# Kernel optimization log

Hardware: AMD Instinct MI355X
Metric: run time of the kernel (lower is better)

## Reference

```python
import jax, jax.numpy as jnp
import numpy as np

NOISE_STD = 0.05
ALPHA = 0.2

B, T, I, H, O, R = 64, 1024, 8, 512, 2, 2


def setup_inputs() -> dict:
    key = jax.random.key(0)
    ks = jax.random.split(key, 6)
    return {
        "input": jax.random.normal(ks[0], (B, T, I), dtype=jnp.float32),
        "noise": jax.random.normal(ks[1], (B, T, H), dtype=jnp.float32),
        "wi": jax.random.normal(ks[2], (I, H), dtype=jnp.float32),
        "si": jnp.ones((I,), dtype=jnp.float32),
        "m": jax.random.normal(ks[3], (H, R), dtype=jnp.float32),
        "n": jax.random.normal(ks[4], (H, R), dtype=jnp.float32),
        "wo": jax.random.normal(ks[5], (H, O), dtype=jnp.float32) * 4.0,
        "so": jnp.ones((O,), dtype=jnp.float32),
        "h0": jnp.zeros((H,), dtype=jnp.float32),
    }


def reference(input, noise, wi, si, m, n, wo, so, h0):
    batch, seq_len, _ = input.shape
    hidden = m.shape[0]
    wi_full = wi * si[:, None]          # (I, H)
    wo_full = wo * so                   # (H, O)
    # Precompute input projection for all timesteps: (B, T, H)
    inp_proj = jnp.einsum('bti,ih->bth', input, wi_full)
    h_init = jnp.broadcast_to(h0, (batch, hidden))
    r_init = jnp.tanh(h_init)

    def step(carry, xs):
        h, r = carry
        nz, p = xs  # (B, H) each
        rec = (r @ n) @ m.T / hidden    # rank-r recurrent drive
        h = h + NOISE_STD * nz + ALPHA * (-h + rec + p)
        r = jnp.tanh(h)
        out = r @ wo_full / hidden      # (B, O)
        return (h, r), (out, h)

    xs = (jnp.swapaxes(noise, 0, 1), jnp.swapaxes(inp_proj, 0, 1))  # time-major
    _, (output, traj) = jax.lax.scan(step, (h_init, r_init), xs)
    return jnp.swapaxes(output, 0, 1), jnp.swapaxes(traj, 0, 1)
```

## Files before the change

kernel.cpp:

```cpp
#include <hip/hip_runtime.h>
#include <cstddef>

constexpr int B = 64, T = 1024, I = 8, H = 512, O = 2;
constexpr float ALPHA = 0.2f;
constexpr float NOISE_STD = 0.05f;

constexpr int PF = 8;

template <int CTRL>
__device__ __forceinline__ float dpp_add(float x) {
    int y = __builtin_amdgcn_update_dpp(0, __float_as_int(x), CTRL, 0xF, 0xF, true);
    return x + __int_as_float(y);
}

__device__ __forceinline__ float wave_sum_to_lane63(float x) {
    x = dpp_add<0x111>(x);
    x = dpp_add<0x112>(x);
    x = dpp_add<0x114>(x);
    x = dpp_add<0x118>(x);
    x = dpp_add<0x142>(x);
    x = dpp_add<0x143>(x);
    return x;
}

__device__ __forceinline__ float fast_tanh(float x) {
    float z = __builtin_amdgcn_exp2f(x * 2.885390081777927f);
    return fmaf(-2.0f, __builtin_amdgcn_rcpf(z + 1.0f), 1.0f);
}

__global__ __launch_bounds__(256)
void rnn_fused4_kernel(const float* __restrict__ input,
                       const float* __restrict__ noise,
                       const float* __restrict__ wi,
                       const float* __restrict__ si,
                       const float* __restrict__ m,
                       const float* __restrict__ n,
                       const float* __restrict__ wo,
                       const float* __restrict__ so,
                       const float* __restrict__ h0,
                       float* __restrict__ out,
                       float* __restrict__ traj)
{
    const int b    = blockIdx.x;
    const int w    = threadIdx.x >> 6;
    const int lane = threadIdx.x & 63;
    const int j0   = w * 128 + 2 * lane;

    __shared__ float  xin[T * I];
    __shared__ float4 part[2][4];

    {
        const float4* src = (const float4*)(input + (size_t)b * T * I);
        float4*       dst = (float4*)xin;
#pragma unroll
        for (int i = 0; i < (T * I / 4) / 256; ++i)
            dst[threadIdx.x + 256 * i] = src[threadIdx.x + 256 * i];
    }
    __syncthreads();

    constexpr float RS  = ALPHA / (float)H;
    constexpr float OMA = 1.0f - ALPHA;
    const float so0 = so[0] / (float)H;
    const float so1 = so[1] / (float)H;

    const float4 mv = *(const float4*)(m + 2 * j0);
    const float4 nv = *(const float4*)(n + 2 * j0);
    const float4 wv = *(const float4*)(wo + 2 * j0);
    const float mm0[2] = {mv.x * RS, mv.z * RS};
    const float mm1[2] = {mv.y * RS, mv.w * RS};
    const float nn0[2] = {nv.x, nv.z};
    const float nn1[2] = {nv.y, nv.w};
    const float ww0[2] = {wv.x, wv.z};
    const float ww1[2] = {wv.y, wv.w};

    float wif[I][2];
#pragma unroll
    for (int i = 0; i < I; ++i) {
        wif[i][0] = wi[i * H + j0]     * si[i];
        wif[i][1] = wi[i * H + j0 + 1] * si[i];
    }

    const float2 h0v = *(const float2*)(h0 + j0);
    float h[2] = {h0v.x, h0v.y};
    float r[2] = {tanhf(h[0]), tanhf(h[1])};

    const float* pn   = noise + (size_t)b * T * H + j0;
    float*       pt   = traj  + (size_t)b * T * H + j0;
    float*       pout = out   + (size_t)b * T * O;

    float2 ring[PF];
#pragma unroll
    for (int u = 0; u < PF; ++u) ring[u] = *(const float2*)(pn + (size_t)u * H);

    static_assert(T % PF == 0, "T must be a multiple of PF");

    for (int tb = 0; tb < T; tb += PF) {
#pragma unroll
        for (int u = 0; u < PF; ++u) {
            const int t = tb + u;

            const float4 xa = *(const float4*)(xin + t * I);
            const float4 xb = *(const float4*)(xin + t * I + 4);

            float pa0 = fmaf(r[1], nn0[1], r[0] * nn0[0]);
            float pa1 = fmaf(r[1], nn1[1], r[0] * nn1[0]);
            float po0 = fmaf(r[1], ww0[1], r[0] * ww0[0]);
            float po1 = fmaf(r[1], ww1[1], r[0] * ww1[0]);

            const float2 nz = ring[u];
            if (t + PF < T) ring[u] = *(const float2*)(pn + (size_t)(t + PF) * H);

            pa0 = wave_sum_to_lane63(pa0);
            pa1 = wave_sum_to_lane63(pa1);
            po0 = wave_sum_to_lane63(po0);
            po1 = wave_sum_to_lane63(po1);

            const float x0 = xa.x, x1 = xa.y, x2 = xa.z, x3 = xa.w;
            const float x4 = xb.x, x5 = xb.y, x6 = xb.z, x7 = xb.w;
            float acc0 = x0 * wif[0][0], acc1 = x0 * wif[0][1];
            acc0 = fmaf(x1, wif[1][0], acc0); acc1 = fmaf(x1, wif[1][1], acc1);
            acc0 = fmaf(x2, wif[2][0], acc0); acc1 = fmaf(x2, wif[2][1], acc1);
            acc0 = fmaf(x3, wif[3][0], acc0); acc1 = fmaf(x3, wif[3][1], acc1);
            acc0 = fmaf(x4, wif[4][0], acc0); acc1 = fmaf(x4, wif[4][1], acc1);
            acc0 = fmaf(x5, wif[5][0], acc0); acc1 = fmaf(x5, wif[5][1], acc1);
            acc0 = fmaf(x6, wif[6][0], acc0); acc1 = fmaf(x6, wif[6][1], acc1);
            acc0 = fmaf(x7, wif[7][0], acc0); acc1 = fmaf(x7, wif[7][1], acc1);
            const float dv0 = fmaf(NOISE_STD, nz.x, ALPHA * acc0);
            const float dv1 = fmaf(NOISE_STD, nz.y, ALPHA * acc1);
            const float pre0 = fmaf(h[0], OMA, dv0);
            const float pre1 = fmaf(h[1], OMA, dv1);

            if (lane == 63) part[t & 1][w] = make_float4(pa0, pa1, po0, po1);

            __builtin_amdgcn_sched_barrier(0);
            asm volatile("s_waitcnt lgkmcnt(0)" ::: "memory");
            __builtin_amdgcn_s_barrier();
            __builtin_amdgcn_sched_barrier(0);

            const float4 q0 = part[t & 1][0];
            const float4 q1 = part[t & 1][1];
            const float4 q2 = part[t & 1][2];
            const float4 q3 = part[t & 1][3];
            const float a0 = (q0.x + q1.x) + (q2.x + q3.x);
            const float a1 = (q0.y + q1.y) + (q2.y + q3.y);

            if (t > 0 && threadIdx.x == 63) {
                const float o0 = (q0.z + q1.z) + (q2.z + q3.z);
                const float o1 = (q0.w + q1.w) + (q2.w + q3.w);
                *(float2*)(pout + (size_t)(t - 1) * O) =
                    make_float2(o0 * so0, o1 * so1);
            }

            h[0] = fmaf(a1, mm1[0], fmaf(a0, mm0[0], pre0));
            h[1] = fmaf(a1, mm1[1], fmaf(a0, mm0[1], pre1));
            r[0] = fast_tanh(h[0]);
            r[1] = fast_tanh(h[1]);

            *(float2*)(pt + (size_t)t * H) = make_float2(h[0], h[1]);
        }
    }

    {
        float po0 = fmaf(r[1], ww0[1], r[0] * ww0[0]);
        float po1 = fmaf(r[1], ww1[1], r[0] * ww1[0]);
        po0 = wave_sum_to_lane63(po0);
        po1 = wave_sum_to_lane63(po1);
        if (lane == 63) part[0][w] = make_float4(po0, po1, 0.f, 0.f);
        __syncthreads();
        if (threadIdx.x == 0) {
            const float4 q0 = part[0][0];
            const float4 q1 = part[0][1];
            const float4 q2 = part[0][2];
            const float4 q3 = part[0][3];
            const float o0 = (q0.x + q1.x) + (q2.x + q3.x);
            const float o1 = (q0.y + q1.y) + (q2.y + q3.y);
            *(float2*)(pout + (size_t)(T - 1) * O) =
                make_float2(o0 * so0, o1 * so1);
        }
    }
}

extern "C" void kernel_launch(void* const* d_in, const int* in_sizes, int n_in,
                              void* d_out, int out_size, void* d_ws, size_t ws_size,
                              hipStream_t stream) {
    const float* input = (const float*)d_in[0];
    const float* noise = (const float*)d_in[1];
    const float* wi    = (const float*)d_in[2];
    const float* si    = (const float*)d_in[3];
    const float* m     = (const float*)d_in[4];
    const float* n     = (const float*)d_in[5];
    const float* wo    = (const float*)d_in[6];
    const float* so    = (const float*)d_in[7];
    const float* h0    = (const float*)d_in[8];

    float* out  = (float*)d_out;
    float* traj = (float*)d_out + (size_t)B * T * O;

    (void)d_ws; (void)ws_size;

    rnn_fused4_kernel<<<B, 256, 0, stream>>>(input, noise, wi, si,
                                             m, n, wo, so, h0, out, traj);
}
```

Before: 560.9 us.

## Process two batch rows per block to share per-step barrier latency

Each 256-thread block now advances two independent batch recurrences in lockstep, so the grid has half as many blocks. The wave reductions, LDS partial exchange and single per-step barrier are shared by two chains, which adds instruction-level parallelism to hide the latency of the serial time loop. In exchange, each block does double the per-step ALU and memory work, uses more registers, and fewer CUs are active. Clamped prefetch indices remove branches, and the output for step t-1 is written from a wrapped index; the bogus write at t=0 lands on T-1 and is overwritten after the loop.

```diff
diff --git a/kernel.cpp b/kernel.cpp
--- a/kernel.cpp
+++ b/kernel.cpp
@@ -6,6 +6,7 @@
 constexpr float NOISE_STD = 0.05f;
 
 constexpr int PF = 8;
+constexpr int NB = 2;
 
 template <int CTRL>
 __device__ __forceinline__ float dpp_add(float x) {
@@ -29,31 +30,31 @@
 }
 
 __global__ __launch_bounds__(256)
-void rnn_fused4_kernel(const float* __restrict__ input,
-                       const float* __restrict__ noise,
-                       const float* __restrict__ wi,
-                       const float* __restrict__ si,
-                       const float* __restrict__ m,
-                       const float* __restrict__ n,
-                       const float* __restrict__ wo,
-                       const float* __restrict__ so,
-                       const float* __restrict__ h0,
-                       float* __restrict__ out,
-                       float* __restrict__ traj)
+void rnn_dual_kernel(const float* __restrict__ input,
+                     const float* __restrict__ noise,
+                     const float* __restrict__ wi,
+                     const float* __restrict__ si,
+                     const float* __restrict__ m,
+                     const float* __restrict__ n,
+                     const float* __restrict__ wo,
+                     const float* __restrict__ so,
+                     const float* __restrict__ h0,
+                     float* __restrict__ out,
+                     float* __restrict__ traj)
 {
-    const int b    = blockIdx.x;
+    const int b0   = blockIdx.x * NB;
     const int w    = threadIdx.x >> 6;
     const int lane = threadIdx.x & 63;
     const int j0   = w * 128 + 2 * lane;
 
-    __shared__ float  xin[T * I];
-    __shared__ float4 part[2][4];
+    __shared__ float  xin[NB * T * I];
+    __shared__ float4 part[2][NB][4];
 
     {
-        const float4* src = (const float4*)(input + (size_t)b * T * I);
+        const float4* src = (const float4*)(input + (size_t)b0 * T * I);
         float4*       dst = (float4*)xin;
 #pragma unroll
-        for (int i = 0; i < (T * I / 4) / 256; ++i)
+        for (int i = 0; i < (NB * T * I / 4) / 256; ++i)
             dst[threadIdx.x + 256 * i] = src[threadIdx.x + 256 * i];
     }
     __syncthreads();
@@ -81,101 +82,146 @@
     }
 
     const float2 h0v = *(const float2*)(h0 + j0);
-    float h[2] = {h0v.x, h0v.y};
-    float r[2] = {tanhf(h[0]), tanhf(h[1])};
-
-    const float* pn   = noise + (size_t)b * T * H + j0;
-    float*       pt   = traj  + (size_t)b * T * H + j0;
-    float*       pout = out   + (size_t)b * T * O;
-
-    float2 ring[PF];
-#pragma unroll
-    for (int u = 0; u < PF; ++u) ring[u] = *(const float2*)(pn + (size_t)u * H);
+    float h[NB][2], r[NB][2];
+#pragma unroll
+    for (int q = 0; q < NB; ++q) {
+        h[q][0] = h0v.x;        h[q][1] = h0v.y;
+        r[q][0] = tanhf(h0v.x); r[q][1] = tanhf(h0v.y);
+    }
+
+    const float* pn[NB];
+    float*       pt[NB];
+    float*       pout[NB];
+#pragma unroll
+    for (int q = 0; q < NB; ++q) {
+        pn[q]   = noise + (size_t)(b0 + q) * T * H + j0;
+        pt[q]   = traj  + (size_t)(b0 + q) * T * H + j0;
+        pout[q] = out   + (size_t)(b0 + q) * T * O;
+    }
+
+    float2 ring[NB][PF];
+#pragma unroll
+    for (int u = 0; u < PF; ++u)
+#pragma unroll
+        for (int q = 0; q < NB; ++q)
+            ring[q][u] = *(const float2*)(pn[q] + (size_t)u * H);
 
     static_assert(T % PF == 0, "T must be a multiple of PF");
 
     for (int tb = 0; tb < T; tb += PF) {
 #pragma unroll
         for (int u = 0; u < PF; ++u) {
-            const int t = tb + u;
-
-            const float4 xa = *(const float4*)(xin + t * I);
-            const float4 xb = *(const float4*)(xin + t * I + 4);
-
-            float pa0 = fmaf(r[1], nn0[1], r[0] * nn0[0]);
-            float pa1 = fmaf(r[1], nn1[1], r[0] * nn1[0]);
-            float po0 = fmaf(r[1], ww0[1], r[0] * ww0[0]);
-            float po1 = fmaf(r[1], ww1[1], r[0] * ww1[0]);
-
-            const float2 nz = ring[u];
-            if (t + PF < T) ring[u] = *(const float2*)(pn + (size_t)(t + PF) * H);
-
-            pa0 = wave_sum_to_lane63(pa0);
-            pa1 = wave_sum_to_lane63(pa1);
-            po0 = wave_sum_to_lane63(po0);
-            po1 = wave_sum_to_lane63(po1);
-
-            const float x0 = xa.x, x1 = xa.y, x2 = xa.z, x3 = xa.w;
-            const float x4 = xb.x, x5 = xb.y, x6 = xb.z, x7 = xb.w;
-            float acc0 = x0 * wif[0][0], acc1 = x0 * wif[0][1];
-            acc0 = fmaf(x1, wif[1][0], acc0); acc1 = fmaf(x1, wif[1][1], acc1);
-            acc0 = fmaf(x2, wif[2][0], acc0); acc1 = fmaf(x2, wif[2][1], acc1);
-            acc0 = fmaf(x3, wif[3][0], acc0); acc1 = fmaf(x3, wif[3][1], acc1);
-            acc0 = fmaf(x4, wif[4][0], acc0); acc1 = fmaf(x4, wif[4][1], acc1);
-            acc0 = fmaf(x5, wif[5][0], acc0); acc1 = fmaf(x5, wif[5][1], acc1);
-            acc0 = fmaf(x6, wif[6][0], acc0); acc1 = fmaf(x6, wif[6][1], acc1);
-            acc0 = fmaf(x7, wif[7][0], acc0); acc1 = fmaf(x7, wif[7][1], acc1);
-            const float dv0 = fmaf(NOISE_STD, nz.x, ALPHA * acc0);
-            const float dv1 = fmaf(NOISE_STD, nz.y, ALPHA * acc1);
-            const float pre0 = fmaf(h[0], OMA, dv0);
-            const float pre1 = fmaf(h[1], OMA, dv1);
-
-            if (lane == 63) part[t & 1][w] = make_float4(pa0, pa1, po0, po1);
+            const int t  = tb + u;
+            const int tn = (t + PF < T) ? (t + PF) : (T - 1);
+
+            float pa0[NB], pa1[NB], po0[NB], po1[NB];
+#pragma unroll
+            for (int q = 0; q < NB; ++q) {
+                pa0[q] = fmaf(r[q][1], nn0[1], r[q][0] * nn0[0]);
+                pa1[q] = fmaf(r[q][1], nn1[1], r[q][0] * nn1[0]);
+                po0[q] = fmaf(r[q][1], ww0[1], r[q][0] * ww0[0]);
+                po1[q] = fmaf(r[q][1], ww1[1], r[q][0] * ww1[0]);
+            }
+
+            float2 nz[NB];
+#pragma unroll
+            for (int q = 0; q < NB; ++q) {
+                nz[q]      = ring[q][u];
+                ring[q][u] = *(const float2*)(pn[q] + (size_t)tn * H);
+            }
+
+#pragma unroll
+            for (int q = 0; q < NB; ++q) {
+                pa0[q] = wave_sum_to_lane63(pa0[q]);
+                pa1[q] = wave_sum_to_lane63(pa1[q]);
+                po0[q] = wave_sum_to_lane63(po0[q]);
+                po1[q] = wave_sum_to_lane63(po1[q]);
+            }
+
+            float pre[NB][2];
+#pragma unroll
+            for (int q = 0; q < NB; ++q) {
+                const float4 xa = *(const float4*)(xin + (q * T + t) * I);
+                const float4 xb = *(const float4*)(xin + (q * T + t) * I + 4);
+                float a0 = xa.x * wif[0][0], a1 = xa.x * wif[0][1];
+                a0 = fmaf(xa.y, wif[1][0], a0); a1 = fmaf(xa.y, wif[1][1], a1);
+                a0 = fmaf(xa.z, wif[2][0], a0); a1 = fmaf(xa.z, wif[2][1], a1);
+                a0 = fmaf(xa.w, wif[3][0], a0); a1 = fmaf(xa.w, wif[3][1], a1);
+                a0 = fmaf(xb.x, wif[4][0], a0); a1 = fmaf(xb.x, wif[4][1], a1);
+                a0 = fmaf(xb.y, wif[5][0], a0); a1 = fmaf(xb.y, wif[5][1], a1);
+                a0 = fmaf(xb.z, wif[6][0], a0); a1 = fmaf(xb.z, wif[6][1], a1);
+                a0 = fmaf(xb.w, wif[7][0], a0); a1 = fmaf(xb.w, wif[7][1], a1);
+                const float dv0 = fmaf(NOISE_STD, nz[q].x, ALPHA * a0);
+                const float dv1 = fmaf(NOISE_STD, nz[q].y, ALPHA * a1);
+                pre[q][0] = fmaf(h[q][0], OMA, dv0);
+                pre[q][1] = fmaf(h[q][1], OMA, dv1);
+            }
+
+            if (lane == 63) {
+#pragma unroll
+                for (int q = 0; q < NB; ++q)
+                    part[t & 1][q][w] = make_float4(pa0[q], pa1[q], po0[q], po1[q]);
+            }
 
             __builtin_amdgcn_sched_barrier(0);
             asm volatile("s_waitcnt lgkmcnt(0)" ::: "memory");
             __builtin_amdgcn_s_barrier();
             __builtin_amdgcn_sched_barrier(0);
 
-            const float4 q0 = part[t & 1][0];
-            const float4 q1 = part[t & 1][1];
-            const float4 q2 = part[t & 1][2];
-            const float4 q3 = part[t & 1][3];
-            const float a0 = (q0.x + q1.x) + (q2.x + q3.x);
-            const float a1 = (q0.y + q1.y) + (q2.y + q3.y);
-
-            if (t > 0 && threadIdx.x == 63) {
-                const float o0 = (q0.z + q1.z) + (q2.z + q3.z);
-                const float o1 = (q0.w + q1.w) + (q2.w + q3.w);
-                *(float2*)(pout + (size_t)(t - 1) * O) =
+#pragma unroll
+            for (int q = 0; q < NB; ++q) {
+                const float4 q0 = part[t & 1][q][0];
+                const float4 q1 = part[t & 1][q][1];
+                const float4 q2 = part[t & 1][q][2];
+                const float4 q3 = part[t & 1][q][3];
+                const float a0 = (q0.x + q1.x) + (q2.x + q3.x);
+                const float a1 = (q0.y + q1.y) + (q2.y + q3.y);
+
+                if (lane == 63) {
+                    const float o0 = (q0.z + q1.z) + (q2.z + q3.z);
+                    const float o1 = (q0.w + q1.w) + (q2.w + q3.w);
+                    const int tm1 = (t + T - 1) & (T - 1);
+                    *(float2*)(pout[q] + (size_t)tm1 * O) =
+                        make_float2(o0 * so0, o1 * so1);
+                }
+
+                h[q][0] = fmaf(a1, mm1[0], fmaf(a0, mm0[0], pre[q][0]));
+                h[q][1] = fmaf(a1, mm1[1], fmaf(a0, mm0[1], pre[q][1]));
+                r[q][0] = fast_tanh(h[q][0]);
+                r[q][1] = fast_tanh(h[q][1]);
+
+                *(float2*)(pt[q] + (size_t)t * H) = make_float2(h[q][0], h[q][1]);
+            }
+        }
+    }
+
+    {
+        float p0[NB], p1[NB];
+#pragma unroll
+        for (int q = 0; q < NB; ++q) {
+            p0[q] = fmaf(r[q][1], ww0[1], r[q][0] * ww0[0]);
+            p1[q] = fmaf(r[q][1], ww1[1], r[q][0] * ww1[0]);
+            p0[q] = wave_sum_to_lane63(p0[q]);
+            p1[q] = wave_sum_to_lane63(p1[q]);
+        }
+        if (lane == 63) {
+#pragma unroll
+            for (int q = 0; q < NB; ++q)
+                part[0][q][w] = make_float4(p0[q], p1[q], 0.f, 0.f);
+        }
+        __syncthreads();
+        if (lane == 63) {
+#pragma unroll
+            for (int q = 0; q < NB; ++q) {
+                const float4 q0 = part[0][q][0];
+                const float4 q1 = part[0][q][1];
+                const float4 q2 = part[0][q][2];
+                const float4 q3 = part[0][q][3];
+                const float o0 = (q0.x + q1.x) + (q2.x + q3.x);
+                const float o1 = (q0.y + q1.y) + (q2.y + q3.y);
+                *(float2*)(pout[q] + (size_t)(T - 1) * O) =
                     make_float2(o0 * so0, o1 * so1);
             }
-
-            h[0] = fmaf(a1, mm1[0], fmaf(a0, mm0[0], pre0));
-            h[1] = fmaf(a1, mm1[1], fmaf(a0, mm0[1], pre1));
-            r[0] = fast_tanh(h[0]);
-            r[1] = fast_tanh(h[1]);
-
-            *(float2*)(pt + (size_t)t * H) = make_float2(h[0], h[1]);
-        }
-    }
-
-    {
-        float po0 = fmaf(r[1], ww0[1], r[0] * ww0[0]);
-        float po1 = fmaf(r[1], ww1[1], r[0] * ww1[0]);
-        po0 = wave_sum_to_lane63(po0);
-        po1 = wave_sum_to_lane63(po1);
-        if (lane == 63) part[0][w] = make_float4(po0, po1, 0.f, 0.f);
-        __syncthreads();
-        if (threadIdx.x == 0) {
-            const float4 q0 = part[0][0];
-            const float4 q1 = part[0][1];
-            const float4 q2 = part[0][2];
-            const float4 q3 = part[0][3];
-            const float o0 = (q0.x + q1.x) + (q2.x + q3.x);
-            const float o1 = (q0.y + q1.y) + (q2.y + q3.y);
-            *(float2*)(pout + (size_t)(T - 1) * O) =
-                make_float2(o0 * so0, o1 * so1);
         }
     }
 }
@@ -198,6 +244,6 @@
 
     (void)d_ws; (void)ws_size;
 
-    rnn_fused4_kernel<<<B, 256, 0, stream>>>(input, noise, wi, si,
-                                             m, n, wo, so, h0, out, traj);
-}
+    rnn_dual_kernel<<<B / NB, 256, 0, stream>>>(input, noise, wi, si,
+                                                m, n, wo, so, h0, out, traj);
+}
```

Result: slower. 818.1 us (+45.8%).

## Batch global memory traffic into chunk boundaries with double-buffered noise registers

Applied to the files above, without the earlier changes.

Restructures the time loop into pairs of 8-step chunks. Noise is loaded into two alternating register banks at chunk boundaries, and trajectory stores and output writes are buffered and issued together after each chunk rather than inside every barrier-synchronised step. The aim is to keep vector memory instructions and their waitcnts off the serial per-step critical path. The cost is higher register pressure, an extra block barrier per chunk, and output writes staged through shared memory.

```diff
diff --git a/kernel.cpp b/kernel.cpp
--- a/kernel.cpp
+++ b/kernel.cpp
@@ -5,7 +5,8 @@
 constexpr float ALPHA = 0.2f;
 constexpr float NOISE_STD = 0.05f;
 
-constexpr int PF = 8;
+constexpr int C  = 8;
+constexpr int NC = T / C;
 
 template <int CTRL>
 __device__ __forceinline__ float dpp_add(float x) {
@@ -29,17 +30,17 @@
 }
 
 __global__ __launch_bounds__(256)
-void rnn_fused4_kernel(const float* __restrict__ input,
-                       const float* __restrict__ noise,
-                       const float* __restrict__ wi,
-                       const float* __restrict__ si,
-                       const float* __restrict__ m,
-                       const float* __restrict__ n,
-                       const float* __restrict__ wo,
-                       const float* __restrict__ so,
-                       const float* __restrict__ h0,
-                       float* __restrict__ out,
-                       float* __restrict__ traj)
+void rnn_chunk_kernel(const float* __restrict__ input,
+                      const float* __restrict__ noise,
+                      const float* __restrict__ wi,
+                      const float* __restrict__ si,
+                      const float* __restrict__ m,
+                      const float* __restrict__ n,
+                      const float* __restrict__ wo,
+                      const float* __restrict__ so,
+                      const float* __restrict__ h0,
+                      float* __restrict__ out,
+                      float* __restrict__ traj)
 {
     const int b    = blockIdx.x;
     const int w    = threadIdx.x >> 6;
@@ -48,6 +49,7 @@
 
     __shared__ float  xin[T * I];
     __shared__ float4 part[2][4];
+    __shared__ float2 obuf[C];
 
     {
         const float4* src = (const float4*)(input + (size_t)b * T * I);
@@ -88,76 +90,105 @@
     float*       pt   = traj  + (size_t)b * T * H + j0;
     float*       pout = out   + (size_t)b * T * O;
 
-    float2 ring[PF];
-#pragma unroll
-    for (int u = 0; u < PF; ++u) ring[u] = *(const float2*)(pn + (size_t)u * H);
-
-    static_assert(T % PF == 0, "T must be a multiple of PF");
-
-    for (int tb = 0; tb < T; tb += PF) {
-#pragma unroll
-        for (int u = 0; u < PF; ++u) {
-            const int t = tb + u;
-
-            const float4 xa = *(const float4*)(xin + t * I);
-            const float4 xb = *(const float4*)(xin + t * I + 4);
-
-            float pa0 = fmaf(r[1], nn0[1], r[0] * nn0[0]);
-            float pa1 = fmaf(r[1], nn1[1], r[0] * nn1[0]);
-            float po0 = fmaf(r[1], ww0[1], r[0] * ww0[0]);
-            float po1 = fmaf(r[1], ww1[1], r[0] * ww1[0]);
-
-            const float2 nz = ring[u];
-            if (t + PF < T) ring[u] = *(const float2*)(pn + (size_t)(t + PF) * H);
-
-            pa0 = wave_sum_to_lane63(pa0);
-            pa1 = wave_sum_to_lane63(pa1);
-            po0 = wave_sum_to_lane63(po0);
-            po1 = wave_sum_to_lane63(po1);
-
-            const float x0 = xa.x, x1 = xa.y, x2 = xa.z, x3 = xa.w;
-            const float x4 = xb.x, x5 = xb.y, x6 = xb.z, x7 = xb.w;
-            float acc0 = x0 * wif[0][0], acc1 = x0 * wif[0][1];
-            acc0 = fmaf(x1, wif[1][0], acc0); acc1 = fmaf(x1, wif[1][1], acc1);
-            acc0 = fmaf(x2, wif[2][0], acc0); acc1 = fmaf(x2, wif[2][1], acc1);
-            acc0 = fmaf(x3, wif[3][0], acc0); acc1 = fmaf(x3, wif[3][1], acc1);
-            acc0 = fmaf(x4, wif[4][0], acc0); acc1 = fmaf(x4, wif[4][1], acc1);
-            acc0 = fmaf(x5, wif[5][0], acc0); acc1 = fmaf(x5, wif[5][1], acc1);
-            acc0 = fmaf(x6, wif[6][0], acc0); acc1 = fmaf(x6, wif[6][1], acc1);
-            acc0 = fmaf(x7, wif[7][0], acc0); acc1 = fmaf(x7, wif[7][1], acc1);
-            const float dv0 = fmaf(NOISE_STD, nz.x, ALPHA * acc0);
-            const float dv1 = fmaf(NOISE_STD, nz.y, ALPHA * acc1);
-            const float pre0 = fmaf(h[0], OMA, dv0);
-            const float pre1 = fmaf(h[1], OMA, dv1);
-
-            if (lane == 63) part[t & 1][w] = make_float4(pa0, pa1, po0, po1);
-
-            __builtin_amdgcn_sched_barrier(0);
-            asm volatile("s_waitcnt lgkmcnt(0)" ::: "memory");
-            __builtin_amdgcn_s_barrier();
-            __builtin_amdgcn_sched_barrier(0);
-
-            const float4 q0 = part[t & 1][0];
-            const float4 q1 = part[t & 1][1];
-            const float4 q2 = part[t & 1][2];
-            const float4 q3 = part[t & 1][3];
-            const float a0 = (q0.x + q1.x) + (q2.x + q3.x);
-            const float a1 = (q0.y + q1.y) + (q2.y + q3.y);
-
-            if (t > 0 && threadIdx.x == 63) {
-                const float o0 = (q0.z + q1.z) + (q2.z + q3.z);
-                const float o1 = (q0.w + q1.w) + (q2.w + q3.w);
-                *(float2*)(pout + (size_t)(t - 1) * O) =
-                    make_float2(o0 * so0, o1 * so1);
-            }
-
-            h[0] = fmaf(a1, mm1[0], fmaf(a0, mm0[0], pre0));
-            h[1] = fmaf(a1, mm1[1], fmaf(a0, mm0[1], pre1));
-            r[0] = fast_tanh(h[0]);
-            r[1] = fast_tanh(h[1]);
-
-            *(float2*)(pt + (size_t)t * H) = make_float2(h[0], h[1]);
-        }
+    float2 nzA[C], nzB[C];
+    float2 hhA[C], hhB[C];
+
+#pragma unroll
+    for (int u = 0; u < C; ++u) nzA[u] = *(const float2*)(pn + (size_t)u * H);
+#pragma unroll
+    for (int u = 0; u < C; ++u) nzB[u] = *(const float2*)(pn + (size_t)(C + u) * H);
+
+    auto do_step = [&](const int t, const int u, const float2 nzv, float2& hslot) {
+        const float4 xa = *(const float4*)(xin + t * I);
+        const float4 xb = *(const float4*)(xin + t * I + 4);
+
+        float pa0 = fmaf(r[1], nn0[1], r[0] * nn0[0]);
+        float pa1 = fmaf(r[1], nn1[1], r[0] * nn1[0]);
+        float po0 = fmaf(r[1], ww0[1], r[0] * ww0[0]);
+        float po1 = fmaf(r[1], ww1[1], r[0] * ww1[0]);
+
+        pa0 = wave_sum_to_lane63(pa0);
+        pa1 = wave_sum_to_lane63(pa1);
+        po0 = wave_sum_to_lane63(po0);
+        po1 = wave_sum_to_lane63(po1);
+
+        float acc0 = xa.x * wif[0][0], acc1 = xa.x * wif[0][1];
+        acc0 = fmaf(xa.y, wif[1][0], acc0); acc1 = fmaf(xa.y, wif[1][1], acc1);
+        acc0 = fmaf(xa.z, wif[2][0], acc0); acc1 = fmaf(xa.z, wif[2][1], acc1);
+        acc0 = fmaf(xa.w, wif[3][0], acc0); acc1 = fmaf(xa.w, wif[3][1], acc1);
+        acc0 = fmaf(xb.x, wif[4][0], acc0); acc1 = fmaf(xb.x, wif[4][1], acc1);
+        acc0 = fmaf(xb.y, wif[5][0], acc0); acc1 = fmaf(xb.y, wif[5][1], acc1);
+        acc0 = fmaf(xb.z, wif[6][0], acc0); acc1 = fmaf(xb.z, wif[6][1], acc1);
+        acc0 = fmaf(xb.w, wif[7][0], acc0); acc1 = fmaf(xb.w, wif[7][1], acc1);
+        const float dv0  = fmaf(NOISE_STD, nzv.x, ALPHA * acc0);
+        const float dv1  = fmaf(NOISE_STD, nzv.y, ALPHA * acc1);
+        const float pre0 = fmaf(h[0], OMA, dv0);
+        const float pre1 = fmaf(h[1], OMA, dv1);
+
+        if (lane == 63) part[u & 1][w] = make_float4(pa0, pa1, po0, po1);
+
+        __builtin_amdgcn_sched_barrier(0);
+        asm volatile("s_waitcnt lgkmcnt(0)" ::: "memory");
+        __builtin_amdgcn_s_barrier();
+        __builtin_amdgcn_sched_barrier(0);
+
+        const float4 q0 = part[u & 1][0];
+        const float4 q1 = part[u & 1][1];
+        const float4 q2 = part[u & 1][2];
+        const float4 q3 = part[u & 1][3];
+        const float a0 = (q0.x + q1.x) + (q2.x + q3.x);
+        const float a1 = (q0.y + q1.y) + (q2.y + q3.y);
+
+        if (threadIdx.x == 63) {
+            const float o0 = (q0.z + q1.z) + (q2.z + q3.z);
+            const float o1 = (q0.w + q1.w) + (q2.w + q3.w);
+            obuf[u] = make_float2(o0 * so0, o1 * so1);
+        }
+
+        h[0] = fmaf(a1, mm1[0], fmaf(a0, mm0[0], pre0));
+        h[1] = fmaf(a1, mm1[1], fmaf(a0, mm0[1], pre1));
+        r[0] = fast_tanh(h[0]);
+        r[1] = fast_tanh(h[1]);
+
+        hslot = make_float2(h[0], h[1]);
+    };
+
+    auto boundary = [&](const int t0, float2 (&nz)[C], float2 (&hh)[C]) {
+#pragma unroll
+        for (int u = 0; u < C; ++u) {
+            const int tl = t0 + 2 * C + u;
+            const int tc = (tl < T) ? tl : (T - 1);
+            nz[u] = *(const float2*)(pn + (size_t)tc * H);
+        }
+#pragma unroll
+        for (int u = 0; u < C; ++u)
+            *(float2*)(pt + (size_t)(t0 + u) * H) = hh[u];
+
+        __builtin_amdgcn_sched_barrier(0);
+        asm volatile("s_waitcnt lgkmcnt(0)" ::: "memory");
+        __builtin_amdgcn_s_barrier();
+        __builtin_amdgcn_sched_barrier(0);
+        if (threadIdx.x < C) {
+            const float2 ov = obuf[threadIdx.x];
+            const int    t  = t0 + (int)threadIdx.x - 1;
+            if (t >= 0) *(float2*)(pout + (size_t)t * O) = ov;
+        }
+    };
+
+    static_assert(NC % 2 == 0, "chunk count must be even");
+
+#pragma unroll 1
+    for (int tc = 0; tc < NC; tc += 2) {
+        const int base0 = tc * C;
+        const int base1 = base0 + C;
+
+#pragma unroll
+        for (int u = 0; u < C; ++u) do_step(base0 + u, u, nzA[u], hhA[u]);
+        boundary(base0, nzA, hhA);
+
+#pragma unroll
+        for (int u = 0; u < C; ++u) do_step(base1 + u, u, nzB[u], hhB[u]);
+        boundary(base1, nzB, hhB);
     }
 
     {
@@ -167,7 +198,7 @@
         po1 = wave_sum_to_lane63(po1);
         if (lane == 63) part[0][w] = make_float4(po0, po1, 0.f, 0.f);
         __syncthreads();
-        if (threadIdx.x == 0) {
+        if (threadIdx.x == 63) {
             const float4 q0 = part[0][0];
             const float4 q1 = part[0][1];
             const float4 q2 = part[0][2];
@@ -198,6 +229,6 @@
 
     (void)d_ws; (void)ws_size;
 
-    rnn_fused4_kernel<<<B, 256, 0, stream>>>(input, noise, wi, si,
-                                             m, n, wo, so, h0, out, traj);
-}
+    rnn_chunk_kernel<<<B, 256, 0, stream>>>(input, noise, wi, si,
+                                            m, n, wo, so, h0, out, traj);
+}
```

Result: no change. 570.5 us (+1.7%).
